# Optimization experiments

Measured on AMD Instinct MI355X. Metric: run time of the kernel, lower is better.

The kernel has to match this reference:

```python
import jax, jax.numpy as jnp
import numpy as np

IN_SIZE = 128
OUT_SIZE = 128
NEG_SLOPE = 0.01  # flax.nnx.leaky_relu default negative_slope


def setup_inputs() -> dict:
    key = jax.random.key(0)
    x = jax.random.normal(key, (16, IN_SIZE, IN_SIZE, 128), dtype=jnp.float32)
    return {"x": x}


def reference(x) -> jnp.ndarray:
    B, _, _, C = x.shape
    up = jax.image.resize(x, (B, 2 * IN_SIZE, 2 * IN_SIZE, C), method='bilinear', antialias=False)
    # leaky_relu activation on the enlarged intermediate
    act = jnp.where(up >= 0, up, NEG_SLOPE * up)
    # bilinear downsample back to out_size (antialias=False, matching original)
    out = jax.image.resize(act, (B, OUT_SIZE, OUT_SIZE, C), method='bilinear', antialias=False)
    return out
```

## Files before the change

kernel.cpp:

```cpp
#include <hip/hip_runtime.h>


#define NEG_SLOPE 0.01f

__device__ __forceinline__ float lrelu(float v) {
    return fmaxf(v, NEG_SLOPE * v);
}

__device__ __forceinline__ float stencil(float a, float b, float c,
                                         float d, float e, float f,
                                         float g, float h, float i) {
    float up00 = 0.5625f * e + 0.1875f * (b + d) + 0.0625f * a;
    float up01 = 0.5625f * e + 0.1875f * (b + f) + 0.0625f * c;
    float up10 = 0.5625f * e + 0.1875f * (d + h) + 0.0625f * g;
    float up11 = 0.5625f * e + 0.1875f * (f + h) + 0.0625f * i;
    return 0.25f * (lrelu(up00) + lrelu(up01) + lrelu(up10) + lrelu(up11));
}

__device__ __forceinline__ float4 stencil4(const float4& a, const float4& b, const float4& c,
                                           const float4& d, const float4& e, const float4& f,
                                           const float4& g, const float4& h, const float4& i) {
    float4 o;
    o.x = stencil(a.x, b.x, c.x, d.x, e.x, f.x, g.x, h.x, i.x);
    o.y = stencil(a.y, b.y, c.y, d.y, e.y, f.y, g.y, h.y, i.y);
    o.z = stencil(a.z, b.z, c.z, d.z, e.z, f.z, g.z, h.z, i.z);
    o.w = stencil(a.w, b.w, c.w, d.w, e.w, f.w, g.w, h.w, i.w);
    return o;
}

__global__ __launch_bounds__(256) void ActivationFilter_kernel(
        const float4* __restrict__ in, float4* __restrict__ out) {
    const int t  = blockIdx.x * 256 + threadIdx.x;
    const int c4 = t & 31;
    const int px = (t >> 5) & 63;
    const int py = (t >> 11) & 63;
    const int b  = t >> 17;

    const int x0 = px << 1, y0 = py << 1;
    const int xm = max(x0 - 1, 0), x3 = min(x0 + 2, 127);
    const int ym = max(y0 - 1, 0), y3 = min(y0 + 2, 127);

    const int rb = b << 7;
#define ADDR(Y, X) (((((rb + (Y)) << 7) + (X)) << 5) + c4)

    const float4 v00 = in[ADDR(ym,   xm)], v01 = in[ADDR(ym,   x0)],
                 v02 = in[ADDR(ym,   x0+1)], v03 = in[ADDR(ym,   x3)];
    const float4 v10 = in[ADDR(y0,   xm)], v11 = in[ADDR(y0,   x0)],
                 v12 = in[ADDR(y0,   x0+1)], v13 = in[ADDR(y0,   x3)];
    const float4 v20 = in[ADDR(y0+1, xm)], v21 = in[ADDR(y0+1, x0)],
                 v22 = in[ADDR(y0+1, x0+1)], v23 = in[ADDR(y0+1, x3)];
    const float4 v30 = in[ADDR(y3,   xm)], v31 = in[ADDR(y3,   x0)],
                 v32 = in[ADDR(y3,   x0+1)], v33 = in[ADDR(y3,   x3)];

    out[ADDR(y0,   x0  )] = stencil4(v00, v01, v02, v10, v11, v12, v20, v21, v22);
    out[ADDR(y0,   x0+1)] = stencil4(v01, v02, v03, v11, v12, v13, v21, v22, v23);
    out[ADDR(y0+1, x0  )] = stencil4(v10, v11, v12, v20, v21, v22, v30, v31, v32);
    out[ADDR(y0+1, x0+1)] = stencil4(v11, v12, v13, v21, v22, v23, v31, v32, v33);
#undef ADDR
}

extern "C" void kernel_launch(void* const* d_in, const int* in_sizes, int n_in,
                              void* d_out, int out_size, void* d_ws, size_t ws_size,
                              hipStream_t stream) {
    const float4* in = (const float4*)d_in[0];
    float4* out = (float4*)d_out;
    ActivationFilter_kernel<<<dim3(8192), dim3(256), 0, stream>>>(in, out);
}
```

Measured before the change: 226.0 us.

## Stage input halo tile in LDS to share stencil loads across threads

Each block now cooperatively loads a 4-row by 18-column by 128-channel input tile, halo included, into shared memory. After a barrier, each thread reads its 4x4 neighborhood from LDS instead of issuing 16 global float4 loads. This cuts redundant global and L2 traffic from overlapping halos. In exchange it adds about 36KB of LDS per block, a __syncthreads, and index division arithmetic, which may lower occupancy.

```diff
diff --git a/kernel.cpp b/kernel.cpp
--- a/kernel.cpp
+++ b/kernel.cpp
@@ -30,28 +30,45 @@
 
 __global__ __launch_bounds__(256) void ActivationFilter_kernel(
         const float4* __restrict__ in, float4* __restrict__ out) {
-    const int t  = blockIdx.x * 256 + threadIdx.x;
-    const int c4 = t & 31;
-    const int px = (t >> 5) & 63;
-    const int py = (t >> 11) & 63;
-    const int b  = t >> 17;
+    __shared__ float4 lds[4][18][32];
 
-    const int x0 = px << 1, y0 = py << 1;
-    const int xm = max(x0 - 1, 0), x3 = min(x0 + 2, 127);
-    const int ym = max(y0 - 1, 0), y3 = min(y0 + 2, 127);
+    const int tid = threadIdx.x;
+    const int blk = blockIdx.x;
+    const int xs  = (blk & 7) << 4;
+    const int py  = (blk >> 3) & 63;
+    const int b   = blk >> 9;
+    const int y0  = py << 1;
+    const int rb  = b << 7;
 
-    const int rb = b << 7;
+    float4* lf = &lds[0][0][0];
+#pragma unroll
+    for (int k = 0; k < 9; ++k) {
+        const int idx  = tid + (k << 8);
+        const int r    = idx / 576;
+        const int rem  = idx - r * 576;
+        const int xcol = rem >> 5;
+        const int c    = rem & 31;
+        const int row  = min(max(y0 - 1 + r, 0), 127);
+        const int col  = min(max(xs - 1 + xcol, 0), 127);
+        lf[idx] = in[((((rb + row) << 7) + col) << 5) + c];
+    }
+    __syncthreads();
+
+    const int c4 = tid & 31;
+    const int pl = tid >> 5;
+    const int x0 = xs + (pl << 1);
+    const int j0 = pl << 1;
+
+    const float4 v00 = lds[0][j0][c4], v01 = lds[0][j0+1][c4],
+                 v02 = lds[0][j0+2][c4], v03 = lds[0][j0+3][c4];
+    const float4 v10 = lds[1][j0][c4], v11 = lds[1][j0+1][c4],
+                 v12 = lds[1][j0+2][c4], v13 = lds[1][j0+3][c4];
+    const float4 v20 = lds[2][j0][c4], v21 = lds[2][j0+1][c4],
+                 v22 = lds[2][j0+2][c4], v23 = lds[2][j0+3][c4];
+    const float4 v30 = lds[3][j0][c4], v31 = lds[3][j0+1][c4],
+                 v32 = lds[3][j0+2][c4], v33 = lds[3][j0+3][c4];
+
 #define ADDR(Y, X) (((((rb + (Y)) << 7) + (X)) << 5) + c4)
-
-    const float4 v00 = in[ADDR(ym,   xm)], v01 = in[ADDR(ym,   x0)],
-                 v02 = in[ADDR(ym,   x0+1)], v03 = in[ADDR(ym,   x3)];
-    const float4 v10 = in[ADDR(y0,   xm)], v11 = in[ADDR(y0,   x0)],
-                 v12 = in[ADDR(y0,   x0+1)], v13 = in[ADDR(y0,   x3)];
-    const float4 v20 = in[ADDR(y0+1, xm)], v21 = in[ADDR(y0+1, x0)],
-                 v22 = in[ADDR(y0+1, x0+1)], v23 = in[ADDR(y0+1, x3)];
-    const float4 v30 = in[ADDR(y3,   xm)], v31 = in[ADDR(y3,   x0)],
-                 v32 = in[ADDR(y3,   x0+1)], v33 = in[ADDR(y3,   x3)];
-
     out[ADDR(y0,   x0  )] = stencil4(v00, v01, v02, v10, v11, v12, v20, v21, v22);
     out[ADDR(y0,   x0+1)] = stencil4(v01, v02, v03, v11, v12, v13, v21, v22, v23);
     out[ADDR(y0+1, x0  )] = stencil4(v10, v11, v12, v20, v21, v22, v30, v31, v32);
```

After: 225.1 us. No clear change (-0.4%).

## Process four batch images per thread with software-pipelined loads and stores

Applied to the files above, without the earlier changes.

Each thread now handles the same pixel/channel position in four images spaced four apart, with the grid shrunk fourfold. Loads for the next image are issued before computing and storing the current one, so more memory requests are in flight per thread and index arithmetic is shared across images. The cost is higher register pressure (up to 32 float4 values live at once), which can lower occupancy.

```diff
diff --git a/kernel.cpp b/kernel.cpp
--- a/kernel.cpp
+++ b/kernel.cpp
@@ -28,35 +28,71 @@
     return o;
 }
 
+#define LOAD_SET(S, P)                                                        \
+    const float4 S##00 = (P)[o00], S##01 = (P)[o01], S##02 = (P)[o02],        \
+                 S##03 = (P)[o03],                                            \
+                 S##10 = (P)[o10], S##11 = (P)[o11], S##12 = (P)[o12],        \
+                 S##13 = (P)[o13],                                            \
+                 S##20 = (P)[o20], S##21 = (P)[o21], S##22 = (P)[o22],        \
+                 S##23 = (P)[o23],                                            \
+                 S##30 = (P)[o30], S##31 = (P)[o31], S##32 = (P)[o32],        \
+                 S##33 = (P)[o33];
+
+#define CSTORE_SET(S, Q)                                                      \
+    (Q)[s00] = stencil4(S##00, S##01, S##02, S##10, S##11, S##12,             \
+                        S##20, S##21, S##22);                                 \
+    (Q)[s01] = stencil4(S##01, S##02, S##03, S##11, S##12, S##13,             \
+                        S##21, S##22, S##23);                                 \
+    (Q)[s10] = stencil4(S##10, S##11, S##12, S##20, S##21, S##22,             \
+                        S##30, S##31, S##32);                                 \
+    (Q)[s11] = stencil4(S##11, S##12, S##13, S##21, S##22, S##23,             \
+                        S##31, S##32, S##33);
+
 __global__ __launch_bounds__(256) void ActivationFilter_kernel(
         const float4* __restrict__ in, float4* __restrict__ out) {
     const int t  = blockIdx.x * 256 + threadIdx.x;
     const int c4 = t & 31;
     const int px = (t >> 5) & 63;
     const int py = (t >> 11) & 63;
-    const int b  = t >> 17;
+    const int b0 = t >> 17;
 
     const int x0 = px << 1, y0 = py << 1;
     const int xm = max(x0 - 1, 0), x3 = min(x0 + 2, 127);
     const int ym = max(y0 - 1, 0), y3 = min(y0 + 2, 127);
 
-    const int rb = b << 7;
-#define ADDR(Y, X) (((((rb + (Y)) << 7) + (X)) << 5) + c4)
+#define IOFF(Y, X) (((((Y) << 7) + (X)) << 5) + c4)
+    const int o00 = IOFF(ym, xm),   o01 = IOFF(ym, x0),
+              o02 = IOFF(ym, x0+1), o03 = IOFF(ym, x3);
+    const int o10 = IOFF(y0, xm),   o11 = IOFF(y0, x0),
+              o12 = IOFF(y0, x0+1), o13 = IOFF(y0, x3);
+    const int o20 = IOFF(y0+1, xm),   o21 = IOFF(y0+1, x0),
+              o22 = IOFF(y0+1, x0+1), o23 = IOFF(y0+1, x3);
+    const int o30 = IOFF(y3, xm),   o31 = IOFF(y3, x0),
+              o32 = IOFF(y3, x0+1), o33 = IOFF(y3, x3);
+    const int s00 = IOFF(y0, x0),   s01 = IOFF(y0, x0+1);
+    const int s10 = IOFF(y0+1, x0), s11 = IOFF(y0+1, x0+1);
+#undef IOFF
 
-    const float4 v00 = in[ADDR(ym,   xm)], v01 = in[ADDR(ym,   x0)],
-                 v02 = in[ADDR(ym,   x0+1)], v03 = in[ADDR(ym,   x3)];
-    const float4 v10 = in[ADDR(y0,   xm)], v11 = in[ADDR(y0,   x0)],
-                 v12 = in[ADDR(y0,   x0+1)], v13 = in[ADDR(y0,   x3)];
-    const float4 v20 = in[ADDR(y0+1, xm)], v21 = in[ADDR(y0+1, x0)],
-                 v22 = in[ADDR(y0+1, x0+1)], v23 = in[ADDR(y0+1, x3)];
-    const float4 v30 = in[ADDR(y3,   xm)], v31 = in[ADDR(y3,   x0)],
-                 v32 = in[ADDR(y3,   x0+1)], v33 = in[ADDR(y3,   x3)];
+    const int IMG  = 128 * 128 * 32;
+    const int IMG4 = IMG << 2;
 
-    out[ADDR(y0,   x0  )] = stencil4(v00, v01, v02, v10, v11, v12, v20, v21, v22);
-    out[ADDR(y0,   x0+1)] = stencil4(v01, v02, v03, v11, v12, v13, v21, v22, v23);
-    out[ADDR(y0+1, x0  )] = stencil4(v10, v11, v12, v20, v21, v22, v30, v31, v32);
-    out[ADDR(y0+1, x0+1)] = stencil4(v11, v12, v13, v21, v22, v23, v31, v32, v33);
-#undef ADDR
+    const float4* p0 = in  + b0 * IMG;
+    float4*       q0 = out + b0 * IMG;
+    const float4* p1 = p0 + IMG4;
+    float4*       q1 = q0 + IMG4;
+    const float4* p2 = p1 + IMG4;
+    float4*       q2 = q1 + IMG4;
+    const float4* p3 = p2 + IMG4;
+    float4*       q3 = q2 + IMG4;
+
+    LOAD_SET(A, p0)
+    LOAD_SET(B, p1)
+    CSTORE_SET(A, q0)
+    LOAD_SET(C, p2)
+    CSTORE_SET(B, q1)
+    LOAD_SET(D, p3)
+    CSTORE_SET(C, q2)
+    CSTORE_SET(D, q3)
 }
 
 extern "C" void kernel_launch(void* const* d_in, const int* in_sizes, int n_in,
@@ -64,5 +100,5 @@
                               hipStream_t stream) {
     const float4* in = (const float4*)d_in[0];
     float4* out = (float4*)d_out;
-    ActivationFilter_kernel<<<dim3(8192), dim3(256), 0, stream>>>(in, out);
+    ActivationFilter_kernel<<<dim3(2048), dim3(256), 0, stream>>>(in, out);
 }
```

After: 254.7 us. +12.7%, slower.
